# Kernel tuning notes

Measured on AMD Instinct MI355X. Metric: run time of the kernel, lower is better.

The kernel has to match this reference:

```python
import jax, jax.numpy as jnp
import numpy as np


def _next_pow2(n: int) -> int:
    # matches torch: 2 ** ceil(log2(n))
    return 1 << (int(n) - 1).bit_length()


def setup_inputs() -> dict:
    key = jax.random.key(0)
    k1, k2 = jax.random.split(key)
    B, T, L = 256, 32768, 32768
    x = jax.random.normal(k1, (B, T), dtype=jnp.float32)
    filt = jax.random.normal(k2, (1, L), dtype=jnp.float32)
    return {"x": x, "filt": filt}


def reference(x, filt):
    """EpochedFutureFill.forward: exact causal convolution of x with filt.

    The per-token epoched algorithm (tau-step direct sum + FutureFill FFT
    cache refresh every K steps, cache initialized to zero) computes exactly
    y[b, t] = sum_{s=0}^{min(t, L-1)} filt[0, s] * x[b, t-s].
    We compute it with one FFT-based linear convolution, mirroring the
    float32 FFT math of future_fill().
    """
    B, T = x.shape
    L = filt.shape[-1]
    n_fft = _next_pow2(T + L - 1)
    xf = jnp.fft.rfft(x.astype(jnp.float32), n=n_fft)          # (B, n_fft//2+1)
    wf = jnp.fft.rfft(filt.astype(jnp.float32), n=n_fft)       # (1, n_fft//2+1)
    y = jnp.fft.irfft(xf * wf, n=n_fft)[:, :T]                 # causal lags 0..T-1
    return y.astype(x.dtype)
```

## Files before the change

### kernel.cpp

```cpp
#include <hip/hip_runtime.h>
#include <cstdint>

typedef __attribute__((ext_vector_type(8))) short short8;
typedef __attribute__((ext_vector_type(4))) float floatx4;

#define TWO_PI 6.283185307179586f

__device__ __forceinline__ unsigned short f2bf(float f) {
  union { float f; uint32_t u; } c; c.f = f;
  uint32_t u = c.u;
  u += 0x7FFFu + ((u >> 16) & 1u);
  return (unsigned short)(u >> 16);
}
__device__ __forceinline__ uint32_t packbf(float re, float im) {
  return (uint32_t)f2bf(re) | ((uint32_t)f2bf(im) << 16);
}


__global__ __launch_bounds__(256) void prep_all(
    const float* __restrict__ x, const float* __restrict__ filt,
    unsigned short* __restrict__ A1, unsigned short* __restrict__ A2,
    unsigned short* __restrict__ A3, unsigned short* __restrict__ A4,
    uint32_t* __restrict__ Zp, float2* __restrict__ Gw) {
  const int bid = blockIdx.x;
  const int tid = threadIdx.x;
  const float w256 = TWO_PI / 256.0f;
  if (bid < 3072) {
    int idx = bid * 256 + tid;
    if (idx < 131072) {
      int col = idx & 255, row = idx >> 8;
      int k1 = row >> 1, d = row & 1, r = col >> 1, e = col & 1;
      float th = (float)((k1 * r) & 255) * w256;
      float sn, cs; __sincosf(th, &sn, &cs);
      A1[idx] = f2bf(d == 0 ? (e == 0 ? cs : sn) : (e == 0 ? -sn : cs));
    } else if (idx < 393216) {
      int j = idx - 131072;
      int col = j & 511, row = j >> 9;
      int k2 = row >> 1, d = row & 1, cc = col >> 1, e = col & 1;
      float th = (float)((k2 * cc) & 255) * w256;
      float sn, cs; __sincosf(th, &sn, &cs);
      A2[j] = f2bf(d == 0 ? (e == 0 ? cs : sn) : (e == 0 ? -sn : cs));
    } else if (idx < 655360) {
      int j = idx - 393216;
      int col = j & 511, row = j >> 9;
      int cc = row >> 1, d = row & 1, k2 = col >> 1, e = col & 1;
      float th = (float)((k2 * cc) & 255) * w256;
      float sn, cs; __sincosf(th, &sn, &cs);
      A3[j] = f2bf(d == 0 ? (e == 0 ? cs : -sn) : (e == 0 ? sn : cs));
    } else {
      int j = idx - 655360;
      int col = j & 511, row = j >> 9;
      int r = row >> 1, d = row & 1, k1 = col >> 1, e = col & 1;
      float th = (float)((k1 * r) & 255) * w256;
      float sn, cs; __sincosf(th, &sn, &cs);
      A4[j] = f2bf(d == 0 ? (e == 0 ? cs : -sn) : (e == 0 ? sn : cs));
    }
  } else if (bid < 4096) {
    int b2 = bid - 3072;
    int s = b2 >> 3, rq = b2 & 7;
    const float* x0 = x + (size_t)(2 * s) * 32768;
    const float* x1 = x0 + 32768;
    uint32_t v[16];
    #pragma unroll
    for (int rr = 0; rr < 16; ++rr) {
      int t = tid + 256 * (rq * 16 + rr);
      v[rr] = (uint32_t)f2bf(x0[t]) | ((uint32_t)f2bf(x1[t]) << 16);
    }
    uint32_t* dst = Zp + (size_t)(s * 256 + tid) * 128 + rq * 16;
    #pragma unroll
    for (int j = 0; j < 16; j += 4)
      *(uint4*)(dst + j) = make_uint4(v[j], v[j + 1], v[j + 2], v[j + 3]);
  } else {
    int k1 = bid - 4096, c = tid;
    float ar = 0.f, ai = 0.f;
    for (int r = 0; r < 128; ++r) {
      float v = filt[c + 256 * r];
      float th = (float)((k1 * r) & 255) * w256;
      float sn, cs; __sincosf(th, &sn, &cs);
      ar += v * cs; ai -= v * sn;
    }
    float th = (float)((k1 * c) & 65535) * (TWO_PI / 65536.0f);
    float sn, cs; __sincosf(th, &sn, &cs);
    Gw[(k1 << 8) + c] = make_float2(ar * cs + ai * sn, ai * cs - ar * sn);
  }
}

__global__ __launch_bounds__(256) void prep_wb(const float2* __restrict__ Gw,
                                               float2* __restrict__ WtT) {
  int k1 = blockIdx.x, k2 = threadIdx.x;
  float ar = 0.f, ai = 0.f;
  for (int c = 0; c < 256; ++c) {
    float2 g = Gw[(k1 << 8) + c];
    float th = (float)((k2 * c) & 255) * (TWO_PI / 256.0f);
    float sn, cs; __sincosf(th, &sn, &cs);
    ar += g.x * cs + g.y * sn;
    ai += g.y * cs - g.x * sn;
  }
  WtT[(k2 << 8) + k1] = make_float2(ar, ai);
}

template <int MODE, int KITERS>
__global__ __launch_bounds__(256, 2) void dft_stage(
    const unsigned short* __restrict__ Af,
    const unsigned short* __restrict__ Bd,
    uint32_t* __restrict__ outp,
    float* __restrict__ yout,
    const float2* __restrict__ WtT) {
  __shared__ unsigned short Sm[32768];
  constexpr int KP = KITERS * 64;

  const int mt = blockIdx.x >> 8;
  const int nt = blockIdx.x & 255;
  const int m0 = mt * 128, n0 = nt * 128;

  const int tid = threadIdx.x;
  const int w = tid >> 6, lane = tid & 63;
  const int qlo = lane & 15, qhi = lane >> 4;
  const int wr = w >> 1, wc = w & 1;
  const int r8 = lane >> 3, pl = lane & 7, sj = pl ^ r8, q3 = qlo & 7;

  floatx4 acc[4][4];
  #pragma unroll
  for (int i = 0; i < 4; ++i)
    #pragma unroll
    for (int j = 0; j < 4; ++j) acc[i][j] = (floatx4){0.f, 0.f, 0.f, 0.f};

  auto issue = [&](int it, int buf) {
    const int k0 = it * 64;
    unsigned short* Asb = Sm + buf * 8192;
    unsigned short* Bsb = Sm + 16384 + buf * 8192;
    #pragma unroll
    for (int q = 0; q < 4; ++q) {
      const int R = w * 32 + q * 8 + r8;
      const unsigned short* gA = Af + (size_t)(m0 + R) * KP + k0 + sj * 8;
      const unsigned short* gB = Bd + (size_t)(n0 + R) * KP + k0 + sj * 8;
      __builtin_amdgcn_global_load_lds(
          (const __attribute__((address_space(1))) uint32_t*)gA,
          (__attribute__((address_space(3))) uint32_t*)&Asb[(w * 32 + q * 8) * 64], 16, 0, 0);
      __builtin_amdgcn_global_load_lds(
          (const __attribute__((address_space(1))) uint32_t*)gB,
          (__attribute__((address_space(3))) uint32_t*)&Bsb[(w * 32 + q * 8) * 64], 16, 0, 0);
    }
  };

  issue(0, 0);
  for (int it = 0; it < KITERS; ++it) {
    __syncthreads();
    if (it + 1 < KITERS) issue(it + 1, (it + 1) & 1);
    const unsigned short* Ab = Sm + (it & 1) * 8192;
    const unsigned short* Bb = Sm + 16384 + (it & 1) * 8192;
    #pragma unroll
    for (int ks = 0; ks < 2; ++ks) {
      short8 a[4], bb[4];
      #pragma unroll
      for (int im = 0; im < 4; ++im) {
        const int R = wr * 64 + im * 16 + qlo;
        a[im] = *(const short8*)&Ab[R * 64 + (((ks * 4 + qhi) ^ q3) << 3)];
      }
      #pragma unroll
      for (int in = 0; in < 4; ++in) {
        const int R = wc * 64 + in * 16 + qlo;
        bb[in] = *(const short8*)&Bb[R * 64 + (((ks * 4 + qhi) ^ q3) << 3)];
      }
      #pragma unroll
      for (int im = 0; im < 4; ++im)
        #pragma unroll
        for (int in = 0; in < 4; ++in)
          acc[im][in] = __builtin_amdgcn_mfma_f32_16x16x32_bf16(a[im], bb[in], acc[im][in], 0, 0, 0);
    }
  }

  const int s_idx = n0 >> 8;
  const int cl0 = n0 & 255;

  if (MODE == 2) {
    __syncthreads();
    uint32_t* Tr = (uint32_t*)Sm;
    #pragma unroll
    for (int im = 0; im < 4; ++im) {
      const int mloc = wr * 32 + im * 8 + qhi * 2;
      #pragma unroll
      for (int in = 0; in < 4; ++in) {
        const int nloc = wc * 64 + in * 16 + qlo;
        #pragma unroll
        for (int pp = 0; pp < 2; ++pp) {
          const int mC = (m0 >> 1) + mloc + pp;
          float re = acc[im][in][2 * pp], iv = acc[im][in][2 * pp + 1];
          float2 wv = WtT[(mC << 8) + cl0 + nloc];
          float r2 = re * wv.x - iv * wv.y, i2 = re * wv.y + iv * wv.x;
          Tr[nloc * 68 + mloc + pp] = packbf(r2, i2);
        }
      }
    }
    __syncthreads();
    const int ln = tid >> 1, half = tid & 1;
    uint32_t* dst = outp + (size_t)((s_idx << 8) + cl0 + ln) * 256 + (m0 >> 1) + half * 32;
    const uint32_t* srcp = Tr + ln * 68 + half * 32;
    #pragma unroll
    for (int j = 0; j < 32; j += 4)
      *(uint4*)(dst + j) = *(const uint4*)(srcp + j);
    return;
  }

  #pragma unroll
  for (int im = 0; im < 4; ++im) {
    const int mloc = wr * 32 + im * 8 + qhi * 2;
    #pragma unroll
    for (int in = 0; in < 4; ++in) {
      const int nloc = wc * 64 + in * 16 + qlo;
      const int cloc = cl0 + nloc;
      #pragma unroll
      for (int pp = 0; pp < 2; ++pp) {
        const int mC = (m0 >> 1) + mloc + pp;
        float re = acc[im][in][2 * pp], iv = acc[im][in][2 * pp + 1];
        if (MODE == 1) {
          float th = (float)((mC * cloc) & 65535) * (TWO_PI / 65536.0f);
          float sn, cs; __sincosf(th, &sn, &cs);
          float r2 = re * cs + iv * sn, i2 = iv * cs - re * sn;
          outp[(size_t)((s_idx << 8) + mC) * 256 + cloc] = packbf(r2, i2);
        } else if (MODE == 3) {
          float th = (float)((mC * cloc) & 65535) * (TWO_PI / 65536.0f);
          float sn, cs; __sincosf(th, &sn, &cs);
          float r2 = re * cs - iv * sn, i2 = iv * cs + re * sn;
          outp[(size_t)((s_idx << 8) + mC) * 256 + cloc] = packbf(r2, i2);
        } else {
          const float sc = 1.0f / 65536.0f;
          float* y0 = yout + ((size_t)s_idx << 16) + (mC << 8) + cloc;
          y0[0] = re * sc;
          y0[32768] = iv * sc;
        }
      }
    }
  }
}

extern "C" void kernel_launch(void* const* d_in, const int* in_sizes, int n_in,
                              void* d_out, int out_size, void* d_ws, size_t ws_size,
                              hipStream_t stream) {
  const float* x = (const float*)d_in[0];
  const float* filt = (const float*)d_in[1];
  float* Y = (float*)d_out;

  char* ws = (char*)d_ws;
  unsigned short* A1 = (unsigned short*)(ws + 0);
  unsigned short* A2 = (unsigned short*)(ws + 0x40000);
  unsigned short* A3 = (unsigned short*)(ws + 0xC0000);
  unsigned short* A4 = (unsigned short*)(ws + 0x140000);
  float2* Gw  = (float2*)(ws + 0x180000);
  float2* WtT = (float2*)(ws + 0x200000);
  unsigned short* Zp = (unsigned short*)(ws + (3u << 20));
  unsigned short* G2 = (unsigned short*)(ws + 19922944u);
  unsigned short* P  = (unsigned short*)(ws + 53477376u);
  unsigned short* H2 = (unsigned short*)(ws + (3u << 20));

  hipLaunchKernelGGL(prep_all, dim3(4352), dim3(256), 0, stream,
                     x, filt, A1, A2, A3, A4, (uint32_t*)Zp, Gw);
  hipLaunchKernelGGL(prep_wb, dim3(256), dim3(256), 0, stream, Gw, WtT);

  hipLaunchKernelGGL((dft_stage<1, 4>), dim3(1024), dim3(256), 0, stream,
                     A1, Zp, (uint32_t*)G2, (float*)nullptr, (const float2*)nullptr);
  hipLaunchKernelGGL((dft_stage<2, 8>), dim3(1024), dim3(256), 0, stream,
                     A2, G2, (uint32_t*)P, (float*)nullptr, WtT);
  hipLaunchKernelGGL((dft_stage<3, 8>), dim3(1024), dim3(256), 0, stream,
                     A3, P, (uint32_t*)H2, (float*)nullptr, (const float2*)nullptr);
  hipLaunchKernelGGL((dft_stage<4, 8>), dim3(512), dim3(256), 0, stream,
                     A4, H2, (uint32_t*)nullptr, Y, (const float2*)nullptr);
}
```

Before: 185.5 us.

## Deepen GEMM pipeline to four LDS buffers and tabulate twiddles

The DFT GEMM stages move from a double-buffered 64-wide K loop to a four-buffer, 32-wide K pipeline that keeps three chunks in flight. It uses explicit vmcnt waits and raw barriers, a new paired-row LDS swizzle, and raises MFMA priority with setprio. Per-element sincos twiddles in stages 1 and 3 are replaced by a precomputed float2 table built in the prep kernel. The aim is to hide global-to-LDS latency and cut transcendental work in the epilogues, at the cost of more barriers per K and extra table reads.

```diff
diff --git a/kernel.cpp b/kernel.cpp
--- a/kernel.cpp
+++ b/kernel.cpp
@@ -21,7 +21,8 @@
     const float* __restrict__ x, const float* __restrict__ filt,
     unsigned short* __restrict__ A1, unsigned short* __restrict__ A2,
     unsigned short* __restrict__ A3, unsigned short* __restrict__ A4,
-    uint32_t* __restrict__ Zp, float2* __restrict__ Gw) {
+    uint32_t* __restrict__ Zp, float2* __restrict__ Gw,
+    float2* __restrict__ Tw) {
   const int bid = blockIdx.x;
   const int tid = threadIdx.x;
   const float w256 = TWO_PI / 256.0f;
@@ -70,7 +71,7 @@
     #pragma unroll
     for (int j = 0; j < 16; j += 4)
       *(uint4*)(dst + j) = make_uint4(v[j], v[j + 1], v[j + 2], v[j + 3]);
-  } else {
+  } else if (bid < 4352) {
     int k1 = bid - 4096, c = tid;
     float ar = 0.f, ai = 0.f;
     for (int r = 0; r < 128; ++r) {
@@ -82,6 +83,11 @@
     float th = (float)((k1 * c) & 65535) * (TWO_PI / 65536.0f);
     float sn, cs; __sincosf(th, &sn, &cs);
     Gw[(k1 << 8) + c] = make_float2(ar * cs + ai * sn, ai * cs - ar * sn);
+  } else {
+    int k1 = bid - 4352, c = tid;
+    float th = (float)((k1 * c) & 65535) * (TWO_PI / 65536.0f);
+    float sn, cs; __sincosf(th, &sn, &cs);
+    Tw[(k1 << 8) + c] = make_float2(cs, sn);
   }
 }
 
@@ -99,15 +105,15 @@
   WtT[(k2 << 8) + k1] = make_float2(ar, ai);
 }
 
-template <int MODE, int KITERS>
+template <int MODE, int NCHUNK>
 __global__ __launch_bounds__(256, 2) void dft_stage(
     const unsigned short* __restrict__ Af,
     const unsigned short* __restrict__ Bd,
     uint32_t* __restrict__ outp,
     float* __restrict__ yout,
-    const float2* __restrict__ WtT) {
+    const float2* __restrict__ tab) {
   __shared__ unsigned short Sm[32768];
-  constexpr int KP = KITERS * 64;
+  constexpr int KP = NCHUNK * 32;
 
   const int mt = blockIdx.x >> 8;
   const int nt = blockIdx.x & 255;
@@ -117,7 +123,9 @@
   const int w = tid >> 6, lane = tid & 63;
   const int qlo = lane & 15, qhi = lane >> 4;
   const int wr = w >> 1, wc = w & 1;
-  const int r8 = lane >> 3, pl = lane & 7, sj = pl ^ r8, q3 = qlo & 7;
+  const int lj = lane >> 3;
+  const int g = (lane & 7) ^ lj;
+  const int hsel = g & 1, qk8 = (g >> 1) << 3;
 
   floatx4 acc[4][4];
   #pragma unroll
@@ -125,49 +133,58 @@
     #pragma unroll
     for (int j = 0; j < 4; ++j) acc[i][j] = (floatx4){0.f, 0.f, 0.f, 0.f};
 
-  auto issue = [&](int it, int buf) {
-    const int k0 = it * 64;
-    unsigned short* Asb = Sm + buf * 8192;
-    unsigned short* Bsb = Sm + 16384 + buf * 8192;
-    #pragma unroll
-    for (int q = 0; q < 4; ++q) {
-      const int R = w * 32 + q * 8 + r8;
-      const unsigned short* gA = Af + (size_t)(m0 + R) * KP + k0 + sj * 8;
-      const unsigned short* gB = Bd + (size_t)(n0 + R) * KP + k0 + sj * 8;
+  auto issue = [&](int t) {
+    const int buf = t & 3;
+    const int k0 = t * 32;
+    unsigned short* Asb = Sm + buf * 4096;
+    unsigned short* Bsb = Sm + 16384 + buf * 4096;
+    #pragma unroll
+    for (int q = 0; q < 2; ++q) {
+      const int PL = w * 16 + q * 8;
+      const int R = 2 * (PL + lj) + hsel;
+      const unsigned short* gA = Af + (size_t)(m0 + R) * KP + k0 + qk8;
+      const unsigned short* gB = Bd + (size_t)(n0 + R) * KP + k0 + qk8;
       __builtin_amdgcn_global_load_lds(
           (const __attribute__((address_space(1))) uint32_t*)gA,
-          (__attribute__((address_space(3))) uint32_t*)&Asb[(w * 32 + q * 8) * 64], 16, 0, 0);
+          (__attribute__((address_space(3))) uint32_t*)&Asb[PL * 64], 16, 0, 0);
       __builtin_amdgcn_global_load_lds(
           (const __attribute__((address_space(1))) uint32_t*)gB,
-          (__attribute__((address_space(3))) uint32_t*)&Bsb[(w * 32 + q * 8) * 64], 16, 0, 0);
+          (__attribute__((address_space(3))) uint32_t*)&Bsb[PL * 64], 16, 0, 0);
     }
   };
 
-  issue(0, 0);
-  for (int it = 0; it < KITERS; ++it) {
-    __syncthreads();
-    if (it + 1 < KITERS) issue(it + 1, (it + 1) & 1);
-    const unsigned short* Ab = Sm + (it & 1) * 8192;
-    const unsigned short* Bb = Sm + 16384 + (it & 1) * 8192;
-    #pragma unroll
-    for (int ks = 0; ks < 2; ++ks) {
-      short8 a[4], bb[4];
+  issue(0); issue(1); issue(2);
+  #pragma unroll
+  for (int t = 0; t < NCHUNK; ++t) {
+    const int rem = NCHUNK - 1 - t;
+    if (rem >= 2)      asm volatile("s_waitcnt vmcnt(8)" ::: "memory");
+    else if (rem == 1) asm volatile("s_waitcnt vmcnt(4)" ::: "memory");
+    else               asm volatile("s_waitcnt vmcnt(0)" ::: "memory");
+    __builtin_amdgcn_s_barrier();
+    if (t + 3 < NCHUNK) issue(t + 3);
+    __builtin_amdgcn_sched_barrier(0);
+    const unsigned short* Ab = Sm + (t & 3) * 4096;
+    const unsigned short* Bb = Sm + 16384 + (t & 3) * 4096;
+    short8 a[4], bb[4];
+    #pragma unroll
+    for (int im = 0; im < 4; ++im) {
+      const int R = wr * 64 + im * 16 + qlo;
+      const int P = R >> 1;
+      a[im] = *(const short8*)&Ab[(P << 6) + ((((qhi << 1) | (R & 1)) ^ (P & 7)) << 3)];
+    }
+    #pragma unroll
+    for (int in = 0; in < 4; ++in) {
+      const int R = wc * 64 + in * 16 + qlo;
+      const int P = R >> 1;
+      bb[in] = *(const short8*)&Bb[(P << 6) + ((((qhi << 1) | (R & 1)) ^ (P & 7)) << 3)];
+    }
+    __builtin_amdgcn_s_setprio(1);
+    #pragma unroll
+    for (int im = 0; im < 4; ++im)
       #pragma unroll
-      for (int im = 0; im < 4; ++im) {
-        const int R = wr * 64 + im * 16 + qlo;
-        a[im] = *(const short8*)&Ab[R * 64 + (((ks * 4 + qhi) ^ q3) << 3)];
-      }
-      #pragma unroll
-      for (int in = 0; in < 4; ++in) {
-        const int R = wc * 64 + in * 16 + qlo;
-        bb[in] = *(const short8*)&Bb[R * 64 + (((ks * 4 + qhi) ^ q3) << 3)];
-      }
-      #pragma unroll
-      for (int im = 0; im < 4; ++im)
-        #pragma unroll
-        for (int in = 0; in < 4; ++in)
-          acc[im][in] = __builtin_amdgcn_mfma_f32_16x16x32_bf16(a[im], bb[in], acc[im][in], 0, 0, 0);
-    }
+      for (int in = 0; in < 4; ++in)
+        acc[im][in] = __builtin_amdgcn_mfma_f32_16x16x32_bf16(a[im], bb[in], acc[im][in], 0, 0, 0);
+    __builtin_amdgcn_s_setprio(0);
   }
 
   const int s_idx = n0 >> 8;
@@ -186,7 +203,7 @@
         for (int pp = 0; pp < 2; ++pp) {
           const int mC = (m0 >> 1) + mloc + pp;
           float re = acc[im][in][2 * pp], iv = acc[im][in][2 * pp + 1];
-          float2 wv = WtT[(mC << 8) + cl0 + nloc];
+          float2 wv = tab[(mC << 8) + cl0 + nloc];
           float r2 = re * wv.x - iv * wv.y, i2 = re * wv.y + iv * wv.x;
           Tr[nloc * 68 + mloc + pp] = packbf(r2, i2);
         }
@@ -214,14 +231,12 @@
         const int mC = (m0 >> 1) + mloc + pp;
         float re = acc[im][in][2 * pp], iv = acc[im][in][2 * pp + 1];
         if (MODE == 1) {
-          float th = (float)((mC * cloc) & 65535) * (TWO_PI / 65536.0f);
-          float sn, cs; __sincosf(th, &sn, &cs);
-          float r2 = re * cs + iv * sn, i2 = iv * cs - re * sn;
+          float2 tw = tab[(mC << 8) + cloc];
+          float r2 = re * tw.x + iv * tw.y, i2 = iv * tw.x - re * tw.y;
           outp[(size_t)((s_idx << 8) + mC) * 256 + cloc] = packbf(r2, i2);
         } else if (MODE == 3) {
-          float th = (float)((mC * cloc) & 65535) * (TWO_PI / 65536.0f);
-          float sn, cs; __sincosf(th, &sn, &cs);
-          float r2 = re * cs - iv * sn, i2 = iv * cs + re * sn;
+          float2 tw = tab[(mC << 8) + cloc];
+          float r2 = re * tw.x - iv * tw.y, i2 = iv * tw.x + re * tw.y;
           outp[(size_t)((s_idx << 8) + mC) * 256 + cloc] = packbf(r2, i2);
         } else {
           const float sc = 1.0f / 65536.0f;
@@ -248,21 +263,22 @@
   unsigned short* A4 = (unsigned short*)(ws + 0x140000);
   float2* Gw  = (float2*)(ws + 0x180000);
   float2* WtT = (float2*)(ws + 0x200000);
+  float2* Tw  = (float2*)(ws + 0x280000);
   unsigned short* Zp = (unsigned short*)(ws + (3u << 20));
   unsigned short* G2 = (unsigned short*)(ws + 19922944u);
   unsigned short* P  = (unsigned short*)(ws + 53477376u);
   unsigned short* H2 = (unsigned short*)(ws + (3u << 20));
 
-  hipLaunchKernelGGL(prep_all, dim3(4352), dim3(256), 0, stream,
-                     x, filt, A1, A2, A3, A4, (uint32_t*)Zp, Gw);
+  hipLaunchKernelGGL(prep_all, dim3(4608), dim3(256), 0, stream,
+                     x, filt, A1, A2, A3, A4, (uint32_t*)Zp, Gw, Tw);
   hipLaunchKernelGGL(prep_wb, dim3(256), dim3(256), 0, stream, Gw, WtT);
 
-  hipLaunchKernelGGL((dft_stage<1, 4>), dim3(1024), dim3(256), 0, stream,
-                     A1, Zp, (uint32_t*)G2, (float*)nullptr, (const float2*)nullptr);
-  hipLaunchKernelGGL((dft_stage<2, 8>), dim3(1024), dim3(256), 0, stream,
+  hipLaunchKernelGGL((dft_stage<1, 8>), dim3(1024), dim3(256), 0, stream,
+                     A1, Zp, (uint32_t*)G2, (float*)nullptr, Tw);
+  hipLaunchKernelGGL((dft_stage<2, 16>), dim3(1024), dim3(256), 0, stream,
                      A2, G2, (uint32_t*)P, (float*)nullptr, WtT);
-  hipLaunchKernelGGL((dft_stage<3, 8>), dim3(1024), dim3(256), 0, stream,
-                     A3, P, (uint32_t*)H2, (float*)nullptr, (const float2*)nullptr);
-  hipLaunchKernelGGL((dft_stage<4, 8>), dim3(512), dim3(256), 0, stream,
-                     A4, H2, (uint32_t*)nullptr, Y, (const float2*)nullptr);
-}
+  hipLaunchKernelGGL((dft_stage<3, 16>), dim3(1024), dim3(256), 0, stream,
+                     A3, P, (uint32_t*)H2, (float*)nullptr, Tw);
+  hipLaunchKernelGGL((dft_stage<4, 16>), dim3(512), dim3(256), 0, stream,
+                     A4, H2, (uint32_t*)nullptr, Y, Tw);
+}
```

Result: slower. 205.9 us (+11.0%).
